# Kernel optimization log

Hardware: AMD Instinct MI355X
Metric: run time of the kernel (lower is better)

The kernel has to match this reference:

```python
import jax, jax.numpy as jnp
import numpy as np

WS = 8
NUM_HEADS = 4


def _sine_pos_enc(Hp, Wp, C):
    # LinearPositionEmbeddingSine: coords channel 0 = x (width), 1 = y (height)
    yy, xx = jnp.meshgrid(jnp.arange(Hp, dtype=jnp.float32),
                          jnp.arange(Wp, dtype=jnp.float32), indexing='ij')
    freq = jnp.arange(C // 4, dtype=jnp.float32) * (3.14 / 200.0)
    cx = xx[..., None] * freq  # [Hp,Wp,C/4]
    cy = yy[..., None] * freq
    return jnp.concatenate([jnp.sin(cx), jnp.cos(cx), jnp.sin(cy), jnp.cos(cy)], axis=-1)


def setup_inputs() -> dict:
    key = jax.random.key(0)
    ks = jax.random.split(key, 6)
    B, N, C = 10, 16384, 128
    s = 0.02
    return {
        'x': jax.random.normal(ks[0], (B, N, C), jnp.float32),
        'Wq': jax.random.normal(ks[1], (C, C), jnp.float32) * s,
        'bq': jnp.zeros((C,), jnp.float32),
        'Wk': jax.random.normal(ks[2], (C, C), jnp.float32) * s,
        'bk': jnp.zeros((C,), jnp.float32),
        'Wv': jax.random.normal(ks[3], (C, C), jnp.float32) * s,
        'bv': jnp.zeros((C,), jnp.float32),
        'Wo': jax.random.normal(ks[4], (C, C), jnp.float32) * s,
        'bo': jnp.zeros((C,), jnp.float32),
        'size_h': 128,
        'size_w': 128,
    }


def reference(x, Wq, bq, Wk, bk, Wv, bv, Wo, bo, size_h, size_w):
    ws, nh = WS, NUM_HEADS
    B, N, C = x.shape
    H, W = int(size_h), int(size_w)
    bn = B // 5
    hd = C // nh
    scale = hd ** -0.5

    xg = x.reshape(B, H, W, C)
    pad_b = (ws - H % ws) % ws
    pad_r = (ws - W % ws) % ws
    xg = jnp.pad(xg, ((0, 0), (0, pad_b), (0, pad_r), (0, 0)))
    Hp, Wp = H + pad_b, W + pad_r
    nh_win, nw_win = Hp // ws, Wp // ws

    enc = _sine_pos_enc(Hp, Wp, C)  # [Hp,Wp,C], identical across batch
    xe = xg + enc

    q = xe @ Wq + bq
    k = xe @ Wk + bk
    v = xg @ Wv + bv
    kv = jnp.concatenate([k, v], axis=-1)  # [B,Hp,Wp,2C]

    # per-group directional shift with edge duplication (torch.cat-based roll)
    up = jnp.concatenate([kv[:bn, ws:], kv[:bn, Hp - ws:]], axis=1)
    down = jnp.concatenate([kv[bn:2 * bn, :ws], kv[bn:2 * bn, :Hp - ws]], axis=1)
    left = jnp.concatenate([kv[2 * bn:3 * bn, :, ws:], kv[2 * bn:3 * bn, :, Wp - ws:]], axis=2)
    right = jnp.concatenate([kv[3 * bn:4 * bn, :, :ws], kv[3 * bn:4 * bn, :, :Wp - ws]], axis=2)
    center = kv[4 * bn:5 * bn]
    kvs = jnp.concatenate([up, down, left, right, center], axis=0)
    k, v = kvs[..., :C], kvs[..., C:]

    def windows(t):
        # [B,Hp,Wp,C] -> [B, n_windows, heads, ws*ws, hd]
        t = t.reshape(B, nh_win, ws, nw_win, ws, nh, hd)
        t = t.transpose(0, 1, 3, 2, 4, 5, 6)
        return t.reshape(B, nh_win * nw_win, ws * ws, nh, hd).transpose(0, 1, 3, 2, 4)

    qw, kw, vw = windows(q), windows(k), windows(v)
    attn = jnp.einsum('bwhqd,bwhkd->bwhqk', qw, kw) * scale
    attn = jax.nn.softmax(attn, axis=-1)
    out = jnp.einsum('bwhqk,bwhkd->bwhqd', attn, vw)

    out = out.transpose(0, 1, 3, 2, 4).reshape(B, nh_win, nw_win, ws, ws, C)
    out = out.transpose(0, 1, 3, 2, 4, 5).reshape(B, Hp, Wp, C)
    out = out[:, :H, :W, :].reshape(B, N, C)
    return out @ Wo + bo
```

## Files before the change

### kernel.cpp

```cpp
#include <hip/hip_runtime.h>
#include <hip/hip_bf16.h>

typedef __hip_bfloat16 bf16;
typedef short bf16x8 __attribute__((ext_vector_type(8)));
typedef float f32x4 __attribute__((ext_vector_type(4)));

static __device__ __forceinline__ unsigned short f2bf(float f) {
    unsigned u = __float_as_uint(f);
    return (unsigned short)((u + 0x7fffu + ((u >> 16) & 1u)) >> 16);
}
static __device__ __forceinline__ unsigned pack2(float lo, float hi) {
    return (((unsigned)f2bf(hi)) << 16) | (unsigned)f2bf(lo);
}

__global__ __launch_bounds__(256) void enc_tables(
    const float* __restrict__ Wq, const float* __restrict__ bq,
    const float* __restrict__ Wk, const float* __restrict__ bk,
    float* __restrict__ EQc, float* __restrict__ EQr,
    float* __restrict__ EKc, float* __restrict__ EKr)
{
    const int c   = blockIdx.x;
    const int ch  = threadIdx.x & 127;
    const int isk = threadIdx.x >> 7;
    const float* W = isk ? Wk : Wq;
    const float* b = isk ? bk : bq;
    const float FSTEP = (float)(3.14 / 200.0);
    float accC = 0.f, accR = 0.f;
    for (int fi = 0; fi < 32; ++fi) {
        float f = (float)fi * FSTEP;
        float a = (float)c * f;
        float s = sinf(a), co = cosf(a);
        accC = fmaf(s,  W[fi * 128 + ch],        accC);
        accC = fmaf(co, W[(32 + fi) * 128 + ch], accC);
        accR = fmaf(s,  W[(64 + fi) * 128 + ch], accR);
        accR = fmaf(co, W[(96 + fi) * 128 + ch], accR);
    }
    accR += b[ch];
    (isk ? EKc : EQc)[c * 128 + ch] = accC;
    (isk ? EKr : EQr)[c * 128 + ch] = accR;
}

__global__ __launch_bounds__(64) void prep_w(
    const float* __restrict__ Wq, const float* __restrict__ Wk,
    const float* __restrict__ Wv, const float* __restrict__ Wo,
    unsigned short* __restrict__ WTf)
{
    const int bid = blockIdx.x;
    const int j = bid >> 5, t16 = (bid >> 2) & 7, ks = bid & 3;
    const int lane = threadIdx.x;
    const int row = t16 * 16 + (lane & 15);
    const int k0 = ks * 32 + (lane >> 4) * 8;
    const float* W = (j == 0) ? Wq : ((j == 1) ? Wk : ((j == 2) ? Wv : Wo));
    unsigned* d32 = (unsigned*)(WTf + (size_t)bid * 512 + lane * 8);
#pragma unroll
    for (int e = 0; e < 4; ++e) {
        float lo = W[(k0 + 2 * e) * 128 + row];
        float hi = W[(k0 + 2 * e + 1) * 128 + row];
        d32[e] = pack2(lo, hi);
    }
}

__global__ __launch_bounds__(256, 4) void qkv_mfma(
    const float* __restrict__ x,
    const unsigned short* __restrict__ WTf,
    const float* __restrict__ EQc, const float* __restrict__ EQr,
    const float* __restrict__ EKc, const float* __restrict__ EKr,
    const float* __restrict__ bv,
    unsigned short* __restrict__ qb, unsigned short* __restrict__ kb,
    unsigned short* __restrict__ vb)
{
    __shared__ unsigned short xs[64 * 128];
    __shared__ float obf[32 * 128];
    const int tid = threadIdx.x;
    const int mb = blockIdx.x;

    const float* xbase = x + (size_t)mb * (64 * 128);
#pragma unroll
    for (int i = 0; i < 4; ++i) {
        int idx = tid + i * 256;
        int m = idx >> 4, c8 = (idx & 15) << 3;
        float4 f0 = *(const float4*)(xbase + m * 128 + c8);
        float4 f1 = *(const float4*)(xbase + m * 128 + c8 + 4);
        unsigned off = (unsigned)(m * 256 + ((c8 * 2) ^ ((m & 7) << 4)));
        unsigned* d = (unsigned*)((char*)xs + off);
        d[0] = pack2(f0.x, f0.y); d[1] = pack2(f0.z, f0.w);
        d[2] = pack2(f1.x, f1.y); d[3] = pack2(f1.z, f1.w);
    }

    const int lane = tid & 63;
    const int wv4  = tid >> 6;
    const int il = lane & 15, g = lane >> 4;
    const int chb = wv4 << 5;
    const int lx = (il & 7) << 4;
    const int rowimg  = (mb >> 1) & 127;
    const int colbase = (mb & 1) * 64;

    __syncthreads();

    for (int nb = 0; nb < 3; ++nb) {
        bf16x8 aw[2][4];
#pragma unroll
        for (int ct = 0; ct < 2; ++ct)
#pragma unroll
            for (int ks = 0; ks < 4; ++ks)
                aw[ct][ks] = *(const bf16x8*)(WTf
                    + (size_t)((nb * 8 + wv4 * 2 + ct) * 4 + ks) * 512 + lane * 8);

        f32x4 acc[4][2] = {};
#pragma unroll
        for (int ks = 0; ks < 4; ++ks) {
            const int kb0 = ks * 64 + g * 16;
#pragma unroll
            for (int mt = 0; mt < 4; ++mt) {
                bf16x8 bx = *(const bf16x8*)((const char*)xs + (mt * 16 + il) * 256 + (kb0 ^ lx));
                acc[mt][0] = __builtin_amdgcn_mfma_f32_16x16x32_bf16(aw[0][ks], bx, acc[mt][0], 0, 0, 0);
                acc[mt][1] = __builtin_amdgcn_mfma_f32_16x16x32_bf16(aw[1][ks], bx, acc[mt][1], 0, 0, 0);
            }
        }

        const float* Ec = (nb == 0) ? EQc : EKc;
        const float* Er = (nb == 0) ? EQr : EKr;
        unsigned short* dstp = (nb == 0) ? qb : ((nb == 1) ? kb : vb);

#pragma unroll
        for (int half = 0; half < 2; ++half) {
            if (nb > 0 || half > 0) __syncthreads();

#pragma unroll
            for (int ct = 0; ct < 2; ++ct) {
                const int ch0 = chb + ct * 16 + (g << 2);
#pragma unroll
                for (int mt2 = 0; mt2 < 2; ++mt2) {
                    const int ml = mt2 * 16 + il;
                    *(f32x4*)(obf + ml * 128 + (ch0 ^ ((ml & 7) << 2))) =
                        acc[half * 2 + mt2][ct];
                }
            }
            __syncthreads();

#pragma unroll
            for (int i = 0; i < 4; ++i) {
                int idx = tid + i * 256;
                int ml = idx >> 5, c4 = (idx & 31) << 2;
                int m = half * 32 + ml;
                f32x4 v = *(const f32x4*)(obf + ml * 128 + (c4 ^ ((ml & 7) << 2)));
                float a0, a1, a2, a3;
                if (nb < 2) {
                    float4 ec = *(const float4*)(Ec + (colbase + m) * 128 + c4);
                    float4 er = *(const float4*)(Er + rowimg * 128 + c4);
                    a0 = ec.x + er.x; a1 = ec.y + er.y;
                    a2 = ec.z + er.z; a3 = ec.w + er.w;
                } else {
                    float4 bvv = *(const float4*)(bv + c4);
                    a0 = bvv.x; a1 = bvv.y; a2 = bvv.z; a3 = bvv.w;
                }
                uint2 o;
                o.x = pack2(v[0] + a0, v[1] + a1);
                o.y = pack2(v[2] + a2, v[3] + a3);
                *(uint2*)(dstp + ((size_t)mb * 64 + m) * 128 + c4) = o;
            }
        }
    }
}

__global__ __launch_bounds__(512) void attn_o_mfma(
    const unsigned short* __restrict__ qb, const unsigned short* __restrict__ kb,
    const unsigned short* __restrict__ vb,
    const unsigned short* __restrict__ WTf, const float* __restrict__ bo,
    float* __restrict__ out)
{
    __shared__ __align__(16) char smem[49152];
    const int QOFF = 0, KOFF = 16384, VOFF = 32768;

    const int w = blockIdx.x;
    const int b = blockIdx.y;
    const int wy = w >> 4, wx = w & 15;
    const int g4 = b >> 1;
    int swy = wy, swx = wx;
    if (g4 == 0)      { if (wy < 15) swy = wy + 1; }
    else if (g4 == 1) { if (wy > 0)  swy = wy - 1; }
    else if (g4 == 2) { if (wx < 15) swx = wx + 1; }
    else if (g4 == 3) { if (wx > 0)  swx = wx - 1; }
    const int tid = threadIdx.x;
    const size_t bbase = (size_t)b * 16384;

#pragma unroll
    for (int i = 0; i < 2; ++i) {
        int idx = tid + i * 512;
        int m = idx >> 4, ci = idx & 15;
        int sw = (ci << 4) ^ ((m & 7) << 4);
        int qt = ((wy * 8 + (m >> 3)) << 7) + (wx << 3) + (m & 7);
        uint4 rq = *(const uint4*)(qb + (bbase + qt) * 128 + ci * 8);
        *(uint4*)(smem + QOFF + m * 256 + sw) = rq;
        int kt = ((swy * 8 + (m >> 3)) << 7) + (swx << 3) + (m & 7);
        uint4 rk = *(const uint4*)(kb + (bbase + kt) * 128 + ci * 8);
        *(uint4*)(smem + KOFF + m * 256 + sw) = rk;
    }
#pragma unroll
    for (int i = 0; i < 2; ++i) {
        int tok = tid & 63, cs = (tid >> 6) + i * 8;
        int c8 = cs << 3;
        int vt = ((swy * 8 + (tok >> 3)) << 7) + (swx << 3) + (tok & 7);
        uint4 rv = *(const uint4*)(vb + (bbase + vt) * 128 + c8);
        unsigned short e[8] = {
            (unsigned short)rv.x, (unsigned short)(rv.x >> 16),
            (unsigned short)rv.y, (unsigned short)(rv.y >> 16),
            (unsigned short)rv.z, (unsigned short)(rv.z >> 16),
            (unsigned short)rv.w, (unsigned short)(rv.w >> 16) };
#pragma unroll
        for (int t2 = 0; t2 < 8; ++t2) {
            int ch = c8 + t2;
            *(unsigned short*)(smem + VOFF + ch * 128 + ((tok * 2) ^ ((ch & 7) << 4))) = e[t2];
        }
    }
    __syncthreads();

    const int lane = tid & 63;
    const int w8 = tid >> 6;
    const int h = w8 >> 1, half = w8 & 1;
    const int il = lane & 15, g = lane >> 4;
    const int lx = (il & 7) << 4;
    const int cb = h * 64 + g * 16;

    bf16x8 ak[4], bq2[2];
#pragma unroll
    for (int mj = 0; mj < 4; ++mj)
        ak[mj] = *(const bf16x8*)(smem + KOFF + (mj * 16 + il) * 256 + (cb ^ lx));
#pragma unroll
    for (int nt = 0; nt < 2; ++nt)
        bq2[nt] = *(const bf16x8*)(smem + QOFF + ((2 * half + nt) * 16 + il) * 256 + (cb ^ lx));
    f32x4 s[4][2] = {};
#pragma unroll
    for (int mj = 0; mj < 4; ++mj)
#pragma unroll
        for (int nt = 0; nt < 2; ++nt)
            s[mj][nt] = __builtin_amdgcn_mfma_f32_16x16x32_bf16(ak[mj], bq2[nt], s[mj][nt], 0, 0, 0);

    const float scale = 0.17677669529663689f;
    float p[4][2][4];
    float csum[2] = {0.f, 0.f};
#pragma unroll
    for (int mj = 0; mj < 4; ++mj)
#pragma unroll
        for (int nt = 0; nt < 2; ++nt)
#pragma unroll
            for (int r = 0; r < 4; ++r) {
                float e = __expf(s[mj][nt][r] * scale);
                p[mj][nt][r] = e;
                csum[nt] += e;
            }
#pragma unroll
    for (int nt = 0; nt < 2; ++nt) {
        csum[nt] += __shfl_xor(csum[nt], 16);
        csum[nt] += __shfl_xor(csum[nt], 32);
    }
    float inv[2] = {1.f / csum[0], 1.f / csum[1]};

    __syncthreads();

    char* pb = smem + h * 8192;
#pragma unroll
    for (int nt = 0; nt < 2; ++nt) {
        int i = (2 * half + nt) * 16 + il;
#pragma unroll
        for (int mj = 0; mj < 4; ++mj) {
            uint2 o;
            o.x = pack2(p[mj][nt][0] * inv[nt], p[mj][nt][1] * inv[nt]);
            o.y = pack2(p[mj][nt][2] * inv[nt], p[mj][nt][3] * inv[nt]);
            *(uint2*)(pb + i * 128 + ((mj * 32 + g * 8) ^ lx)) = o;
        }
    }

    f32x4 apv[2][2] = {};
#pragma unroll
    for (int ks2 = 0; ks2 < 2; ++ks2) {
        bf16x8 av[2], bp[2];
#pragma unroll
        for (int mc = 0; mc < 2; ++mc)
            av[mc] = *(const bf16x8*)(smem + VOFF + (h * 32 + mc * 16 + il) * 128 + ((ks2 * 64 + g * 16) ^ lx));
#pragma unroll
        for (int nt = 0; nt < 2; ++nt)
            bp[nt] = *(const bf16x8*)(pb + ((2 * half + nt) * 16 + il) * 128 + ((ks2 * 64 + g * 16) ^ lx));
#pragma unroll
        for (int mc = 0; mc < 2; ++mc)
#pragma unroll
            for (int nt = 0; nt < 2; ++nt)
                apv[mc][nt] = __builtin_amdgcn_mfma_f32_16x16x32_bf16(av[mc], bp[nt], apv[mc][nt], 0, 0, 0);
    }
    __syncthreads();

#pragma unroll
    for (int nt = 0; nt < 2; ++nt) {
        int i = (2 * half + nt) * 16 + il;
#pragma unroll
        for (int mc = 0; mc < 2; ++mc) {
            int c0 = h * 32 + mc * 16 + (g << 2);
            uint2 o;
            o.x = pack2(apv[mc][nt][0], apv[mc][nt][1]);
            o.y = pack2(apv[mc][nt][2], apv[mc][nt][3]);
            *(uint2*)(smem + VOFF + i * 256 + ((c0 * 2) ^ lx)) = o;
        }
    }
    __syncthreads();

    bf16x8 awo[4];
#pragma unroll
    for (int ks = 0; ks < 4; ++ks)
        awo[ks] = *(const bf16x8*)(WTf + (size_t)((3 * 8 + w8) * 4 + ks) * 512 + lane * 8);
    f32x4 aco[4] = {};
#pragma unroll
    for (int ks = 0; ks < 4; ++ks) {
#pragma unroll
        for (int nt = 0; nt < 4; ++nt) {
            bf16x8 bao = *(const bf16x8*)(smem + VOFF + (nt * 16 + il) * 256 + ((ks * 64 + g * 16) ^ lx));
            aco[nt] = __builtin_amdgcn_mfma_f32_16x16x32_bf16(awo[ks], bao, aco[nt], 0, 0, 0);
        }
    }

    float bov[4];
#pragma unroll
    for (int r = 0; r < 4; ++r) bov[r] = bo[16 * w8 + (g << 2) + r];
#pragma unroll
    for (int nt = 0; nt < 4; ++nt) {
        int i = nt * 16 + il;
        float4 o4;
        o4.x = aco[nt][0] + bov[0];
        o4.y = aco[nt][1] + bov[1];
        o4.z = aco[nt][2] + bov[2];
        o4.w = aco[nt][3] + bov[3];
        *(float4*)(smem + i * 512 + ((w8 * 64 + g * 16) ^ lx)) = o4;
    }
    __syncthreads();

#pragma unroll
    for (int i = 0; i < 4; ++i) {
        int idx = tid + i * 512;
        int m = idx >> 5, cb16 = (idx & 31) << 4;
        float4 o4 = *(const float4*)(smem + m * 512 + (cb16 ^ ((m & 7) << 4)));
        int t2 = ((wy * 8 + (m >> 3)) << 7) + (wx << 3) + (m & 7);
        *(float4*)(out + (bbase + t2) * 128 + (idx & 31) * 4) = o4;
    }
}

extern "C" void kernel_launch(void* const* d_in, const int* in_sizes, int n_in,
                              void* d_out, int out_size, void* d_ws, size_t ws_size,
                              hipStream_t stream)
{
    const float* x  = (const float*)d_in[0];
    const float* Wq = (const float*)d_in[1];
    const float* bq = (const float*)d_in[2];
    const float* Wk = (const float*)d_in[3];
    const float* bk = (const float*)d_in[4];
    const float* Wv = (const float*)d_in[5];
    const float* bv = (const float*)d_in[6];
    const float* Wo = (const float*)d_in[7];
    const float* bo = (const float*)d_in[8];

    char* ws = (char*)d_ws;
    float* EQc = (float*)(ws);
    float* EQr = (float*)(ws + 65536);
    float* EKc = (float*)(ws + 131072);
    float* EKr = (float*)(ws + 196608);
    unsigned short* WTf = (unsigned short*)(ws + 262144);
    unsigned short* qb = (unsigned short*)(ws + 393216);
    unsigned short* kb = (unsigned short*)(ws + 42336256);
    unsigned short* vb = (unsigned short*)(ws + 84279296);
    float* outp = (float*)d_out;

    enc_tables <<<dim3(128),      256, 0, stream>>>(Wq, bq, Wk, bk, EQc, EQr, EKc, EKr);
    prep_w     <<<dim3(128),       64, 0, stream>>>(Wq, Wk, Wv, Wo, WTf);
    qkv_mfma   <<<dim3(2560),     256, 0, stream>>>(x, WTf, EQc, EQr, EKc, EKr, bv, qb, kb, vb);
    attn_o_mfma<<<dim3(256, 10),  512, 0, stream>>>(qb, kb, vb, WTf, bo, outp);
}
```

Before: 105.3 us.

## Fuse Q projection into attention kernel instead of materializing Q

The Q projection moves out of the QKV kernel and into the attention kernel. Each attention block now loads its window's fp32 x tokens, converts them to bf16, runs MFMA against Wq, and adds the positional encoding tables, writing Q directly into shared memory. This removes the global write and reread of the bf16 Q buffer, about 42 MB of traffic each way. In exchange the attention kernel reads fp32 x, twice the bytes of bf16 Q, and does extra MFMA work plus another barrier before the attention stage.

```diff
diff --git a/kernel.cpp b/kernel.cpp
--- a/kernel.cpp
+++ b/kernel.cpp
@@ -63,11 +63,9 @@
 __global__ __launch_bounds__(256, 4) void qkv_mfma(
     const float* __restrict__ x,
     const unsigned short* __restrict__ WTf,
-    const float* __restrict__ EQc, const float* __restrict__ EQr,
     const float* __restrict__ EKc, const float* __restrict__ EKr,
     const float* __restrict__ bv,
-    unsigned short* __restrict__ qb, unsigned short* __restrict__ kb,
-    unsigned short* __restrict__ vb)
+    unsigned short* __restrict__ kb, unsigned short* __restrict__ vb)
 {
     __shared__ unsigned short xs[64 * 128];
     __shared__ float obf[32 * 128];
@@ -97,7 +95,7 @@
 
     __syncthreads();
 
-    for (int nb = 0; nb < 3; ++nb) {
+    for (int nb = 1; nb < 3; ++nb) {
         bf16x8 aw[2][4];
 #pragma unroll
         for (int ct = 0; ct < 2; ++ct)
@@ -118,13 +116,11 @@
             }
         }
 
-        const float* Ec = (nb == 0) ? EQc : EKc;
-        const float* Er = (nb == 0) ? EQr : EKr;
-        unsigned short* dstp = (nb == 0) ? qb : ((nb == 1) ? kb : vb);
+        unsigned short* dstp = (nb == 1) ? kb : vb;
 
 #pragma unroll
         for (int half = 0; half < 2; ++half) {
-            if (nb > 0 || half > 0) __syncthreads();
+            if (!(nb == 1 && half == 0)) __syncthreads();
 
 #pragma unroll
             for (int ct = 0; ct < 2; ++ct) {
@@ -145,9 +141,9 @@
                 int m = half * 32 + ml;
                 f32x4 v = *(const f32x4*)(obf + ml * 128 + (c4 ^ ((ml & 7) << 2)));
                 float a0, a1, a2, a3;
-                if (nb < 2) {
-                    float4 ec = *(const float4*)(Ec + (colbase + m) * 128 + c4);
-                    float4 er = *(const float4*)(Er + rowimg * 128 + c4);
+                if (nb == 1) {
+                    float4 ec = *(const float4*)(EKc + (colbase + m) * 128 + c4);
+                    float4 er = *(const float4*)(EKr + rowimg * 128 + c4);
                     a0 = ec.x + er.x; a1 = ec.y + er.y;
                     a2 = ec.z + er.z; a3 = ec.w + er.w;
                 } else {
@@ -164,9 +160,11 @@
 }
 
 __global__ __launch_bounds__(512) void attn_o_mfma(
-    const unsigned short* __restrict__ qb, const unsigned short* __restrict__ kb,
-    const unsigned short* __restrict__ vb,
-    const unsigned short* __restrict__ WTf, const float* __restrict__ bo,
+    const float* __restrict__ x,
+    const unsigned short* __restrict__ kb, const unsigned short* __restrict__ vb,
+    const unsigned short* __restrict__ WTf,
+    const float* __restrict__ EQc, const float* __restrict__ EQr,
+    const float* __restrict__ bo,
     float* __restrict__ out)
 {
     __shared__ __align__(16) char smem[49152];
@@ -187,11 +185,21 @@
 #pragma unroll
     for (int i = 0; i < 2; ++i) {
         int idx = tid + i * 512;
+        int m = idx >> 4, c8 = (idx & 15) << 3;
+        int qt = ((wy * 8 + (m >> 3)) << 7) + (wx << 3) + (m & 7);
+        const float* s = x + (bbase + qt) * 128 + c8;
+        float4 f0 = *(const float4*)s;
+        float4 f1 = *(const float4*)(s + 4);
+        unsigned off = (unsigned)(m * 256 + ((c8 * 2) ^ ((m & 7) << 4)));
+        unsigned* d = (unsigned*)(smem + QOFF + off);
+        d[0] = pack2(f0.x, f0.y); d[1] = pack2(f0.z, f0.w);
+        d[2] = pack2(f1.x, f1.y); d[3] = pack2(f1.z, f1.w);
+    }
+#pragma unroll
+    for (int i = 0; i < 2; ++i) {
+        int idx = tid + i * 512;
         int m = idx >> 4, ci = idx & 15;
         int sw = (ci << 4) ^ ((m & 7) << 4);
-        int qt = ((wy * 8 + (m >> 3)) << 7) + (wx << 3) + (m & 7);
-        uint4 rq = *(const uint4*)(qb + (bbase + qt) * 128 + ci * 8);
-        *(uint4*)(smem + QOFF + m * 256 + sw) = rq;
         int kt = ((swy * 8 + (m >> 3)) << 7) + (swx << 3) + (m & 7);
         uint4 rk = *(const uint4*)(kb + (bbase + kt) * 128 + ci * 8);
         *(uint4*)(smem + KOFF + m * 256 + sw) = rk;
@@ -217,9 +225,42 @@
 
     const int lane = tid & 63;
     const int w8 = tid >> 6;
-    const int h = w8 >> 1, half = w8 & 1;
     const int il = lane & 15, g = lane >> 4;
     const int lx = (il & 7) << 4;
+
+    {
+        const int tt = w8 & 3;
+        const int chh4 = (w8 >> 2) * 4;
+        const int qtok = tt * 16 + il;
+        bf16x8 bxq[4];
+#pragma unroll
+        for (int ks = 0; ks < 4; ++ks)
+            bxq[ks] = *(const bf16x8*)(smem + QOFF + qtok * 256 + ((ks * 64 + g * 16) ^ lx));
+        f32x4 qacc[4] = {};
+#pragma unroll
+        for (int ct = 0; ct < 4; ++ct)
+#pragma unroll
+            for (int ks = 0; ks < 4; ++ks) {
+                bf16x8 aw = *(const bf16x8*)(WTf + (size_t)((chh4 + ct) * 4 + ks) * 512 + lane * 8);
+                qacc[ct] = __builtin_amdgcn_mfma_f32_16x16x32_bf16(aw, bxq[ks], qacc[ct], 0, 0, 0);
+            }
+        __syncthreads();
+
+        const int imgrow = wy * 8 + (qtok >> 3), imgcol = wx * 8 + (qtok & 7);
+#pragma unroll
+        for (int ct = 0; ct < 4; ++ct) {
+            int ch0 = (chh4 + ct) * 16 + (g << 2);
+            float4 ec = *(const float4*)(EQc + imgcol * 128 + ch0);
+            float4 er = *(const float4*)(EQr + imgrow * 128 + ch0);
+            uint2 o;
+            o.x = pack2(qacc[ct][0] + ec.x + er.x, qacc[ct][1] + ec.y + er.y);
+            o.y = pack2(qacc[ct][2] + ec.z + er.z, qacc[ct][3] + ec.w + er.w);
+            *(uint2*)(smem + QOFF + qtok * 256 + ((ch0 * 2) ^ lx)) = o;
+        }
+    }
+    __syncthreads();
+
+    const int h = w8 >> 1, half = w8 & 1;
     const int cb = h * 64 + g * 16;
 
     bf16x8 ak[4], bq2[2];
@@ -362,13 +403,12 @@
     float* EKc = (float*)(ws + 131072);
     float* EKr = (float*)(ws + 196608);
     unsigned short* WTf = (unsigned short*)(ws + 262144);
-    unsigned short* qb = (unsigned short*)(ws + 393216);
-    unsigned short* kb = (unsigned short*)(ws + 42336256);
-    unsigned short* vb = (unsigned short*)(ws + 84279296);
+    unsigned short* kb = (unsigned short*)(ws + 393216);
+    unsigned short* vb = (unsigned short*)(ws + 42336256);
     float* outp = (float*)d_out;
 
     enc_tables <<<dim3(128),      256, 0, stream>>>(Wq, bq, Wk, bk, EQc, EQr, EKc, EKr);
     prep_w     <<<dim3(128),       64, 0, stream>>>(Wq, Wk, Wv, Wo, WTf);
-    qkv_mfma   <<<dim3(2560),     256, 0, stream>>>(x, WTf, EQc, EQr, EKc, EKr, bv, qb, kb, vb);
-    attn_o_mfma<<<dim3(256, 10),  512, 0, stream>>>(qb, kb, vb, WTf, bo, outp);
-}
+    qkv_mfma   <<<dim3(2560),     256, 0, stream>>>(x, WTf, EKc, EKr, bv, kb, vb);
+    attn_o_mfma<<<dim3(256, 10),  512, 0, stream>>>(x, kb, vb, WTf, EQc, EQr, bo, outp);
+}
```

Result: slower. 108.7 us (+3.2%).
